# Performance work log

Measured on AMD Instinct MI355X. Metric: run time of the kernel, lower is better.

## Reference

```python
import jax, jax.numpy as jnp
import numpy as np

EPS = 1e-10
NCE_T = 0.1
JSD_T = 1.0

def setup_inputs() -> dict:
    key = jax.random.key(0)
    k1, k2, k3, k4, k5 = jax.random.split(key, 5)
    N, D, C = 8192, 128, 1000
    return {
        'fs': jax.random.normal(k1, (N, D), dtype=jnp.float32),
        'ft': jax.random.normal(k2, (N, D), dtype=jnp.float32),
        'logit_s': jax.random.normal(k3, (N, C), dtype=jnp.float32),
        'logit_t': jax.random.normal(k4, (N, C), dtype=jnp.float32),
        'target': jax.random.randint(k5, (N,), 0, 100, dtype=jnp.int64),
    }

def _l2_normalize(x, axis=1, eps=1e-12):
    n = jnp.sqrt(jnp.sum(x * x, axis=axis, keepdims=True))
    return x / jnp.maximum(n, eps)

def _nce_loss(f1, f2, targets):
    f1 = _l2_normalize(f1)
    f2 = _l2_normalize(f2)
    # pos_mask[i,j] = 1 where targets[i] == targets[j] (same class, incl. diagonal)
    pos_mask = (targets[:, None] == targets[None, :]).astype(jnp.float32)  # [N,N]
    neg_mask = 1.0 - pos_mask
    # dist = ||f1_i - f2_j||^2 = 2 - 2 <f1_i, f2_j> for unit vectors -> cos = 1 - 0.5*dist = f1 @ f2.T
    cos = jnp.matmul(f1, f2.T)  # [N,N]
    ps = jax.nn.softmax(cos / NCE_T, axis=1)
    log_pos = -jnp.log(ps + EPS) * pos_mask
    log_neg = -jnp.log(1.0 - ps + EPS) * neg_mask
    row = log_pos.sum(1) / pos_mask.sum(1) + log_neg.sum(1) / neg_mask.sum(1)
    return row.mean()

def _jsd_loss(y_s, y_t):
    N = y_s.shape[0]
    log_ps = jax.nn.log_softmax(y_s / JSD_T, axis=1)
    log_pt = jax.nn.log_softmax(y_t / JSD_T, axis=1)
    pt = jnp.exp(log_pt)
    ps = jnp.exp(log_ps)
    # F.kl_div(input=log_p, target=q, reduction='sum') = sum(q * (log q - log_p))
    kl_st = jnp.sum(pt * (log_pt - log_ps)) * (JSD_T ** 2) / N
    kl_ts = jnp.sum(ps * (log_ps - log_pt)) * (JSD_T ** 2) / N
    return 0.5 * (kl_st + kl_ts)

def reference(fs, ft, logit_s, logit_t, target):
    return _nce_loss(fs, ft, target) + _jsd_loss(logit_s, logit_t)
```

## Files before the change

kernel.cpp:

```cpp
#include <hip/hip_runtime.h>
#include <hip/hip_bf16.h>

#define NN 8192
#define DD 128
#define CC 1000
#define LN2 0.69314718f
#define G_SCALE 14.42695041f
#define NSTRIP 16
#define JPER   512
#define NTILE  8
#define LROW   128
#define GRID_NCE 1024
#define GRID_TOT 3072

typedef short v8s __attribute__((ext_vector_type(8)));
typedef float v4f __attribute__((ext_vector_type(4)));
typedef unsigned short u16;
typedef unsigned int u32;

typedef __attribute__((address_space(1))) const unsigned char ga_t;
typedef __attribute__((address_space(3))) unsigned char la_t;
#define GLOAD_LDS16(g, l) __builtin_amdgcn_global_load_lds((ga_t*)(g), (la_t*)(l), 16, 0, 0)

#if __has_builtin(__builtin_amdgcn_exp2f)
#define EXP2(x) __builtin_amdgcn_exp2f(x)
#else
#define EXP2(x) exp2f(x)
#endif
#if __has_builtin(__builtin_amdgcn_logf)
#define LOG2(x) __builtin_amdgcn_logf(x)
#else
#define LOG2(x) log2f(x)
#endif

static __device__ __forceinline__ float bf2f(u16 u) {
    union { float f; u32 i; } x; x.i = ((u32)u) << 16; return x.f;
}
static __device__ __forceinline__ u16 f2bf(float f) {
    u32 x = __float_as_uint(f);
    return (u16)((x + 0x7FFFu + ((x >> 16) & 1u)) >> 16);
}
static __device__ __forceinline__ float wsum(float v) {
    #pragma unroll
    for (int m = 1; m < 64; m <<= 1) v += __shfl_xor(v, m, 64);
    return v;
}
static __device__ __forceinline__ float wmax(float v) {
    #pragma unroll
    for (int m = 1; m < 64; m <<= 1) v = fmaxf(v, __shfl_xor(v, m, 64));
    return v;
}

__global__ __launch_bounds__(256) void prep_kernel(const void* __restrict__ fs,
                                                   const void* __restrict__ ft,
                                                   const int* __restrict__ traw,
                                                   u16* __restrict__ f1, u16* __restrict__ f2,
                                                   int* __restrict__ tgt32,
                                                   float* __restrict__ sums) {
    int b = blockIdx.x, tid = threadIdx.x;
    int w = tid >> 6, lane = tid & 63;
    if (b < 1024) {
        #pragma unroll
        for (int r = 0; r < 4; r++) {
            int row4 = b * 16 + w * 4 + r;
            const void* src; u16* dst; float gain; int row;
            if (row4 < NN) { src = fs; dst = f1; gain = G_SCALE; row = row4; }
            else           { src = ft; dst = f2; gain = 1.0f;    row = row4 - NN; }
            u32 wb = ((const u32*)src)[(size_t)row * 64 + lane];
            unsigned e = (wb >> 7) & 0xFF;
            int isF32 = (__popcll(__ballot(e >= 100 && e <= 140)) < 32);
            float x0, x1;
            if (isF32) {
                float2 v = ((const float2*)src)[(size_t)row * 64 + lane];
                x0 = v.x; x1 = v.y;
            } else {
                x0 = bf2f((u16)(wb & 0xFFFF));
                x1 = bf2f((u16)(wb >> 16));
            }
            float ss = wsum(x0 * x0 + x1 * x1);
            float sc = gain / fmaxf(sqrtf(ss), 1e-12f);
            u32 outw = (u32)f2bf(x0 * sc) | ((u32)f2bf(x1 * sc) << 16);
            ((u32*)dst)[(size_t)row * 64 + lane] = outw;
        }
    } else {
        int db = b - 1024;
        if (db == 0 && tid < 4) sums[tid] = 0.0f;
        #pragma unroll
        for (int r = 0; r < 4; r++) {
            int idx = db * 1024 + r * 256 + tid;
            int k = (idx >> 1) & 4095;
            int odd = traw[2 * k + 1];
            int is32 = (__ballot(odd != 0) != 0ull);
            int t = (is32 ? traw[idx] : traw[2 * idx]) & 127;
            tgt32[idx] = t;
        }
    }
}

__global__ __launch_bounds__(256) void main_kernel(const u16* __restrict__ f1,
                                                   const u16* __restrict__ f2,
                                                   const int* __restrict__ tgt,
                                                   const void* __restrict__ ls,
                                                   const void* __restrict__ lt,
                                                   float* __restrict__ Pp,
                                                   float* __restrict__ Qp,
                                                   float* __restrict__ Sp,
                                                   float* __restrict__ sums) {
    __shared__ u16 lds[2][64 * LROW];
    __shared__ float sred[4];
    int bx = blockIdx.x;
    int tid = threadIdx.x;
    int w = tid >> 6, lane = tid & 63;

    if (bx < GRID_NCE) {
        int strip = bx & (NSTRIP - 1);
        int ib = bx >> 4;
        int quad = lane >> 4, lcol = lane & 15;
        int ibase = ib * 128 + w * 32;

        v8s a0[4], a1[4];
        #pragma unroll
        for (int t = 0; t < 4; t++) {
            int k = t * 32 + quad * 8;
            a0[t] = *(const v8s*)(f1 + (size_t)(ibase + lcol) * DD + k);
            a1[t] = *(const v8s*)(f1 + (size_t)(ibase + 16 + lcol) * DD + k);
        }
        int ti[8];
        #pragma unroll
        for (int a = 0; a < 2; a++)
            #pragma unroll
            for (int v = 0; v < 4; v++)
                ti[a * 4 + v] = tgt[ibase + a * 16 + quad * 4 + v];

        float P[8] = {}, Q[8] = {}, S[8] = {};

        int rrl = 4 * w + (lane >> 4);
        int cg = (lane & 15) ^ rrl;
        const u16* gb = f2 + (size_t)strip * JPER * DD + (size_t)rrl * DD + cg * 8;
        int ldsbase = 4 * w * 256;

        #pragma unroll
        for (int r = 0; r < 4; r++)
            GLOAD_LDS16(gb + (size_t)r * 16 * DD,
                        (unsigned char*)lds[0] + ldsbase + r * 16 * 256);

        for (int it = 0; it < NTILE; ++it) {
            __syncthreads();
            if (it + 1 < NTILE) {
                const u16* g2 = gb + (size_t)(it + 1) * 64 * DD;
                unsigned char* l2 = (unsigned char*)lds[(it + 1) & 1] + ldsbase;
                #pragma unroll
                for (int r = 0; r < 4; r++)
                    GLOAD_LDS16(g2 + (size_t)r * 16 * DD, l2 + r * 16 * 256);
            }
            int jb = strip * JPER + it * 64;
            int tj0 = tgt[jb + lcol];
            int tj1 = tgt[jb + 16 + lcol];
            int tj2 = tgt[jb + 32 + lcol];
            int tj3 = tgt[jb + 48 + lcol];

            const u16* buf = lds[it & 1];
            v4f zero = {0.f, 0.f, 0.f, 0.f};
            v4f acc[8] = {zero, zero, zero, zero, zero, zero, zero, zero};
            #pragma unroll
            for (int t = 0; t < 4; t++) {
                int s = ((quad + 4 * t) ^ lcol) * 8;
                v8s b0 = *(const v8s*)(buf + (lcol)*LROW + s);
                v8s b1 = *(const v8s*)(buf + (16 + lcol) * LROW + s);
                v8s b2 = *(const v8s*)(buf + (32 + lcol) * LROW + s);
                v8s b3 = *(const v8s*)(buf + (48 + lcol) * LROW + s);
                acc[0] = __builtin_amdgcn_mfma_f32_16x16x32_bf16(a0[t], b0, acc[0], 0, 0, 0);
                acc[1] = __builtin_amdgcn_mfma_f32_16x16x32_bf16(a0[t], b1, acc[1], 0, 0, 0);
                acc[2] = __builtin_amdgcn_mfma_f32_16x16x32_bf16(a0[t], b2, acc[2], 0, 0, 0);
                acc[3] = __builtin_amdgcn_mfma_f32_16x16x32_bf16(a0[t], b3, acc[3], 0, 0, 0);
                acc[4] = __builtin_amdgcn_mfma_f32_16x16x32_bf16(a1[t], b0, acc[4], 0, 0, 0);
                acc[5] = __builtin_amdgcn_mfma_f32_16x16x32_bf16(a1[t], b1, acc[5], 0, 0, 0);
                acc[6] = __builtin_amdgcn_mfma_f32_16x16x32_bf16(a1[t], b2, acc[6], 0, 0, 0);
                acc[7] = __builtin_amdgcn_mfma_f32_16x16x32_bf16(a1[t], b3, acc[7], 0, 0, 0);
            }
            #pragma unroll
            for (int a = 0; a < 2; a++) {
                #pragma unroll
                for (int v = 0; v < 4; v++) {
                    int t_i = ti[a * 4 + v];
                    #pragma unroll
                    for (int jf = 0; jf < 4; jf++) {
                        float s2 = acc[a * 4 + jf][v];
                        float e1 = EXP2(s2);
                        int tj = (jf == 0) ? tj0 : (jf == 1) ? tj1 : (jf == 2) ? tj2 : tj3;
                        bool pos = (tj == t_i);
                        P[a * 4 + v] += e1;
                        Q[a * 4 + v] += pos ? e1 : 0.0f;
                        S[a * 4 + v] += pos ? s2 : 0.0f;
                    }
                }
            }
        }

        #pragma unroll
        for (int a = 0; a < 2; a++) {
            #pragma unroll
            for (int v = 0; v < 4; v++) {
                float p = P[a * 4 + v], q = Q[a * 4 + v], s = S[a * 4 + v];
                #pragma unroll
                for (int m = 1; m < 16; m <<= 1) {
                    p += __shfl_xor(p, m, 64);
                    q += __shfl_xor(q, m, 64);
                    s += __shfl_xor(s, m, 64);
                }
                if (lcol == 0) {
                    size_t idx = (size_t)strip * NN + ibase + a * 16 + quad * 4 + v;
                    Pp[idx] = p;
                    Qp[idx] = q;
                    Sp[idx] = s;
                }
            }
        }
    } else {
        int row = (bx - GRID_NCE) * 4 + w;
        u32 wb = ((const u32*)ls)[(size_t)row * 500 + lane];
        unsigned e = (wb >> 7) & 0xFF;
        int isF32 = (__popcll(__ballot(e >= 100 && e <= 140)) < 32);

        float xs[16], xt[16];
        #pragma unroll
        for (int c = 0; c < 4; c++) {
            int idx = c * 256 + lane * 4;
            if (idx < CC) {
                if (isF32) {
                    float4 a = *(const float4*)((const float*)ls + (size_t)row * CC + idx);
                    float4 b = *(const float4*)((const float*)lt + (size_t)row * CC + idx);
                    xs[c*4+0] = a.x; xs[c*4+1] = a.y; xs[c*4+2] = a.z; xs[c*4+3] = a.w;
                    xt[c*4+0] = b.x; xt[c*4+1] = b.y; xt[c*4+2] = b.z; xt[c*4+3] = b.w;
                } else {
                    ushort4 a = *(const ushort4*)((const u16*)ls + (size_t)row * CC + idx);
                    ushort4 b = *(const ushort4*)((const u16*)lt + (size_t)row * CC + idx);
                    xs[c*4+0] = bf2f(a.x); xs[c*4+1] = bf2f(a.y); xs[c*4+2] = bf2f(a.z); xs[c*4+3] = bf2f(a.w);
                    xt[c*4+0] = bf2f(b.x); xt[c*4+1] = bf2f(b.y); xt[c*4+2] = bf2f(b.z); xt[c*4+3] = bf2f(b.w);
                }
            } else {
                #pragma unroll
                for (int q = 0; q < 4; q++) { xs[c*4+q] = -1e30f; xt[c*4+q] = -1e30f; }
            }
        }
        float ms = -1e30f, mt = -1e30f;
        #pragma unroll
        for (int q = 0; q < 16; q++) { ms = fmaxf(ms, xs[q]); mt = fmaxf(mt, xt[q]); }
        ms = wmax(ms); mt = wmax(mt);
        float es = 0.f, et = 0.f;
        #pragma unroll
        for (int q = 0; q < 16; q++) { es += __expf(xs[q] - ms); et += __expf(xt[q] - mt); }
        es = wsum(es); et = wsum(et);
        float lse_s = ms + __logf(es), lse_t = mt + __logf(et);
        float contrib = 0.f;
        #pragma unroll
        for (int q = 0; q < 16; q++) {
            float lps = xs[q] - lse_s, lpt = xt[q] - lse_t;
            contrib += (lpt - lps) * (__expf(lpt) - __expf(lps));
        }
        contrib = wsum(contrib);
        if (lane == 0) sred[w] = contrib;
        __syncthreads();
        if (tid == 0) atomicAdd(&sums[1], sred[0] + sred[1] + sred[2] + sred[3]);
    }
}

__global__ __launch_bounds__(256) void rowred_kernel(const float* __restrict__ Pp,
                                                     const float* __restrict__ Qp,
                                                     const float* __restrict__ Sp,
                                                     const int* __restrict__ tgt,
                                                     float* __restrict__ sums,
                                                     u32* __restrict__ out) {
    __shared__ int h[128];
    __shared__ float sb[4];
    __shared__ int lastf;
    int tid = threadIdx.x;
    if (tid < 128) h[tid] = 0;
    __syncthreads();
    for (int i = tid; i < NN; i += 256) atomicAdd(&h[tgt[i]], 1);
    __syncthreads();

    int i = blockIdx.x * 256 + tid;
    float P = 0.f, Q = 0.f, S = 0.f;
    #pragma unroll
    for (int s = 0; s < NSTRIP; s++) {
        P += Pp[(size_t)s * NN + i];
        Q += Qp[(size_t)s * NN + i];
        S += Sp[(size_t)s * NN + i];
    }
    int cnt = h[tgt[i]];
    float pos = LN2 * LOG2(P) - LN2 * S / (float)cnt;
    float neg = (1.0f - Q / P) / (float)(NN - cnt);
    float l = wsum(pos + neg);
    if ((tid & 63) == 0) sb[tid >> 6] = l;
    __syncthreads();
    if (tid == 0) {
        atomicAdd(&sums[0], sb[0] + sb[1] + sb[2] + sb[3]);
        __threadfence();
        int* done = (int*)sums + 2;
        lastf = (atomicAdd(done, 1) == 31);
    }
    __syncthreads();
    if (!lastf) return;
    if (tid == 0) {
        float Lsum = __hip_atomic_load(&sums[0], __ATOMIC_RELAXED, __HIP_MEMORY_SCOPE_AGENT);
        float Jsum = __hip_atomic_load(&sums[1], __ATOMIC_RELAXED, __HIP_MEMORY_SCOPE_AGENT);
        float loss = (Lsum + 0.5f * Jsum) / (float)NN;
        u32 fb = __float_as_uint(loss);
        out[0] = (fb & 0xFFFF0000u) | (u32)f2bf(loss);
    }
}

extern "C" void kernel_launch(void* const* d_in, const int* in_sizes, int n_in,
                              void* d_out, int out_size, void* d_ws, size_t ws_size,
                              hipStream_t stream) {
    const void* fs = d_in[0];
    const void* ft = d_in[1];
    const void* ls = d_in[2];
    const void* lt = d_in[3];
    const int* tgt_raw = (const int*)d_in[4];

    char* wsp = (char*)d_ws;
    u16*   f1    = (u16*)(wsp + 0);
    u16*   f2    = (u16*)(wsp + 2097152);
    float* Pp    = (float*)(wsp + 4194304);
    float* Qp    = (float*)(wsp + 4718592);
    float* Sp    = (float*)(wsp + 5242880);
    float* sums  = (float*)(wsp + 5767168);
    int*   tgt32 = (int*)(wsp + 5767424);

    prep_kernel<<<1024 + 8, 256, 0, stream>>>(fs, ft, tgt_raw, f1, f2, tgt32, sums);
    main_kernel<<<GRID_TOT, 256, 0, stream>>>(f1, f2, tgt32, ls, lt, Pp, Qp, Sp, sums);
    rowred_kernel<<<32, 256, 0, stream>>>(Pp, Qp, Sp, tgt32, sums, (u32*)d_out);
}
```

Baseline: 163.5 us.

## Move JSD blocks into prep kernel and build class histogram there

The JSD softmax/KL blocks move out of the NCE matmul kernel and into the prep kernel, so main_kernel launches only the NCE tiles. The target-count histogram is now built in prep via per-block shared histograms merged into a global one, instead of each rowred block rescanning all targets. A hipMemsetAsync zeroes sums and ghist beforehand. This trades an extra memset launch and a longer prep phase for a lighter main kernel and a cheaper rowred, with the risk that the JSD work no longer overlaps the matmul.

```diff
diff --git a/kernel.cpp b/kernel.cpp
--- a/kernel.cpp
+++ b/kernel.cpp
@@ -11,7 +11,8 @@
 #define NTILE  8
 #define LROW   128
 #define GRID_NCE 1024
-#define GRID_TOT 3072
+#define JSD_BLOCKS 2048
+#define PREP_GRID (JSD_BLOCKS + 1024 + 8)
 
 typedef short v8s __attribute__((ext_vector_type(8)));
 typedef float v4f __attribute__((ext_vector_type(4)));
@@ -54,15 +55,68 @@
 __global__ __launch_bounds__(256) void prep_kernel(const void* __restrict__ fs,
                                                    const void* __restrict__ ft,
                                                    const int* __restrict__ traw,
+                                                   const void* __restrict__ ls,
+                                                   const void* __restrict__ lt,
                                                    u16* __restrict__ f1, u16* __restrict__ f2,
                                                    int* __restrict__ tgt32,
+                                                   int* __restrict__ ghist,
                                                    float* __restrict__ sums) {
+    __shared__ float sred[4];
+    __shared__ int h[128];
     int b = blockIdx.x, tid = threadIdx.x;
     int w = tid >> 6, lane = tid & 63;
-    if (b < 1024) {
+
+    if (b < JSD_BLOCKS) {
+        int row = b * 4 + w;
+        u32 wb = ((const u32*)ls)[(size_t)row * 500 + lane];
+        unsigned e = (wb >> 7) & 0xFF;
+        int isF32 = (__popcll(__ballot(e >= 100 && e <= 140)) < 32);
+
+        float xs[16], xt[16];
+        #pragma unroll
+        for (int c = 0; c < 4; c++) {
+            int idx = c * 256 + lane * 4;
+            if (idx < CC) {
+                if (isF32) {
+                    float4 a = *(const float4*)((const float*)ls + (size_t)row * CC + idx);
+                    float4 bb = *(const float4*)((const float*)lt + (size_t)row * CC + idx);
+                    xs[c*4+0] = a.x; xs[c*4+1] = a.y; xs[c*4+2] = a.z; xs[c*4+3] = a.w;
+                    xt[c*4+0] = bb.x; xt[c*4+1] = bb.y; xt[c*4+2] = bb.z; xt[c*4+3] = bb.w;
+                } else {
+                    ushort4 a = *(const ushort4*)((const u16*)ls + (size_t)row * CC + idx);
+                    ushort4 bb = *(const ushort4*)((const u16*)lt + (size_t)row * CC + idx);
+                    xs[c*4+0] = bf2f(a.x); xs[c*4+1] = bf2f(a.y); xs[c*4+2] = bf2f(a.z); xs[c*4+3] = bf2f(a.w);
+                    xt[c*4+0] = bf2f(bb.x); xt[c*4+1] = bf2f(bb.y); xt[c*4+2] = bf2f(bb.z); xt[c*4+3] = bf2f(bb.w);
+                }
+            } else {
+                #pragma unroll
+                for (int q = 0; q < 4; q++) { xs[c*4+q] = -1e30f; xt[c*4+q] = -1e30f; }
+            }
+        }
+        float ms = -1e30f, mt = -1e30f;
+        #pragma unroll
+        for (int q = 0; q < 16; q++) { ms = fmaxf(ms, xs[q]); mt = fmaxf(mt, xt[q]); }
+        ms = wmax(ms); mt = wmax(mt);
+        float es = 0.f, et = 0.f;
+        #pragma unroll
+        for (int q = 0; q < 16; q++) { es += __expf(xs[q] - ms); et += __expf(xt[q] - mt); }
+        es = wsum(es); et = wsum(et);
+        float lse_s = ms + __logf(es), lse_t = mt + __logf(et);
+        float contrib = 0.f;
+        #pragma unroll
+        for (int q = 0; q < 16; q++) {
+            float lps = xs[q] - lse_s, lpt = xt[q] - lse_t;
+            contrib += (lpt - lps) * (__expf(lpt) - __expf(lps));
+        }
+        contrib = wsum(contrib);
+        if (lane == 0) sred[w] = contrib;
+        __syncthreads();
+        if (tid == 0) atomicAdd(&sums[1], sred[0] + sred[1] + sred[2] + sred[3]);
+    } else if (b < JSD_BLOCKS + 1024) {
+        int nb = b - JSD_BLOCKS;
         #pragma unroll
         for (int r = 0; r < 4; r++) {
-            int row4 = b * 16 + w * 4 + r;
+            int row4 = nb * 16 + w * 4 + r;
             const void* src; u16* dst; float gain; int row;
             if (row4 < NN) { src = fs; dst = f1; gain = G_SCALE; row = row4; }
             else           { src = ft; dst = f2; gain = 1.0f;    row = row4 - NN; }
@@ -83,8 +137,9 @@
             ((u32*)dst)[(size_t)row * 64 + lane] = outw;
         }
     } else {
-        int db = b - 1024;
-        if (db == 0 && tid < 4) sums[tid] = 0.0f;
+        int db = b - JSD_BLOCKS - 1024;
+        if (tid < 128) h[tid] = 0;
+        __syncthreads();
         #pragma unroll
         for (int r = 0; r < 4; r++) {
             int idx = db * 1024 + r * 256 + tid;
@@ -93,175 +148,126 @@
             int is32 = (__ballot(odd != 0) != 0ull);
             int t = (is32 ? traw[idx] : traw[2 * idx]) & 127;
             tgt32[idx] = t;
-        }
+            atomicAdd(&h[t], 1);
+        }
+        __syncthreads();
+        if (tid < 128 && h[tid]) atomicAdd(&ghist[tid], h[tid]);
     }
 }
 
 __global__ __launch_bounds__(256) void main_kernel(const u16* __restrict__ f1,
                                                    const u16* __restrict__ f2,
                                                    const int* __restrict__ tgt,
-                                                   const void* __restrict__ ls,
-                                                   const void* __restrict__ lt,
                                                    float* __restrict__ Pp,
                                                    float* __restrict__ Qp,
-                                                   float* __restrict__ Sp,
-                                                   float* __restrict__ sums) {
+                                                   float* __restrict__ Sp) {
     __shared__ u16 lds[2][64 * LROW];
-    __shared__ float sred[4];
     int bx = blockIdx.x;
     int tid = threadIdx.x;
     int w = tid >> 6, lane = tid & 63;
 
-    if (bx < GRID_NCE) {
-        int strip = bx & (NSTRIP - 1);
-        int ib = bx >> 4;
-        int quad = lane >> 4, lcol = lane & 15;
-        int ibase = ib * 128 + w * 32;
-
-        v8s a0[4], a1[4];
+    int strip = bx & (NSTRIP - 1);
+    int ib = bx >> 4;
+    int quad = lane >> 4, lcol = lane & 15;
+    int ibase = ib * 128 + w * 32;
+
+    v8s a0[4], a1[4];
+    #pragma unroll
+    for (int t = 0; t < 4; t++) {
+        int k = t * 32 + quad * 8;
+        a0[t] = *(const v8s*)(f1 + (size_t)(ibase + lcol) * DD + k);
+        a1[t] = *(const v8s*)(f1 + (size_t)(ibase + 16 + lcol) * DD + k);
+    }
+    int ti[8];
+    #pragma unroll
+    for (int a = 0; a < 2; a++)
+        #pragma unroll
+        for (int v = 0; v < 4; v++)
+            ti[a * 4 + v] = tgt[ibase + a * 16 + quad * 4 + v];
+
+    float P[8] = {}, Q[8] = {}, S[8] = {};
+
+    int rrl = 4 * w + (lane >> 4);
+    int cg = (lane & 15) ^ rrl;
+    const u16* gb = f2 + (size_t)strip * JPER * DD + (size_t)rrl * DD + cg * 8;
+    int ldsbase = 4 * w * 256;
+
+    #pragma unroll
+    for (int r = 0; r < 4; r++)
+        GLOAD_LDS16(gb + (size_t)r * 16 * DD,
+                    (unsigned char*)lds[0] + ldsbase + r * 16 * 256);
+
+    for (int it = 0; it < NTILE; ++it) {
+        __syncthreads();
+        if (it + 1 < NTILE) {
+            const u16* g2 = gb + (size_t)(it + 1) * 64 * DD;
+            unsigned char* l2 = (unsigned char*)lds[(it + 1) & 1] + ldsbase;
+            #pragma unroll
+            for (int r = 0; r < 4; r++)
+                GLOAD_LDS16(g2 + (size_t)r * 16 * DD, l2 + r * 16 * 256);
+        }
+        int jb = strip * JPER + it * 64;
+        int tj0 = tgt[jb + lcol];
+        int tj1 = tgt[jb + 16 + lcol];
+        int tj2 = tgt[jb + 32 + lcol];
+        int tj3 = tgt[jb + 48 + lcol];
+
+        const u16* buf = lds[it & 1];
+        v4f zero = {0.f, 0.f, 0.f, 0.f};
+        v4f acc[8] = {zero, zero, zero, zero, zero, zero, zero, zero};
         #pragma unroll
         for (int t = 0; t < 4; t++) {
-            int k = t * 32 + quad * 8;
-            a0[t] = *(const v8s*)(f1 + (size_t)(ibase + lcol) * DD + k);
-            a1[t] = *(const v8s*)(f1 + (size_t)(ibase + 16 + lcol) * DD + k);
-        }
-        int ti[8];
-        #pragma unroll
-        for (int a = 0; a < 2; a++)
-            #pragma unroll
-            for (int v = 0; v < 4; v++)
-                ti[a * 4 + v] = tgt[ibase + a * 16 + quad * 4 + v];
-
-        float P[8] = {}, Q[8] = {}, S[8] = {};
-
-        int rrl = 4 * w + (lane >> 4);
-        int cg = (lane & 15) ^ rrl;
-        const u16* gb = f2 + (size_t)strip * JPER * DD + (size_t)rrl * DD + cg * 8;
-        int ldsbase = 4 * w * 256;
-
-        #pragma unroll
-        for (int r = 0; r < 4; r++)
-            GLOAD_LDS16(gb + (size_t)r * 16 * DD,
-                        (unsigned char*)lds[0] + ldsbase + r * 16 * 256);
-
-        for (int it = 0; it < NTILE; ++it) {
-            __syncthreads();
-            if (it + 1 < NTILE) {
-                const u16* g2 = gb + (size_t)(it + 1) * 64 * DD;
-                unsigned char* l2 = (unsigned char*)lds[(it + 1) & 1] + ldsbase;
-                #pragma unroll
-                for (int r = 0; r < 4; r++)
-                    GLOAD_LDS16(g2 + (size_t)r * 16 * DD, l2 + r * 16 * 256);
-            }
-            int jb = strip * JPER + it * 64;
-            int tj0 = tgt[jb + lcol];
-            int tj1 = tgt[jb + 16 + lcol];
-            int tj2 = tgt[jb + 32 + lcol];
-            int tj3 = tgt[jb + 48 + lcol];
-
-            const u16* buf = lds[it & 1];
-            v4f zero = {0.f, 0.f, 0.f, 0.f};
-            v4f acc[8] = {zero, zero, zero, zero, zero, zero, zero, zero};
-            #pragma unroll
-            for (int t = 0; t < 4; t++) {
-                int s = ((quad + 4 * t) ^ lcol) * 8;
-                v8s b0 = *(const v8s*)(buf + (lcol)*LROW + s);
-                v8s b1 = *(const v8s*)(buf + (16 + lcol) * LROW + s);
-                v8s b2 = *(const v8s*)(buf + (32 + lcol) * LROW + s);
-                v8s b3 = *(const v8s*)(buf + (48 + lcol) * LROW + s);
-                acc[0] = __builtin_amdgcn_mfma_f32_16x16x32_bf16(a0[t], b0, acc[0], 0, 0, 0);
-                acc[1] = __builtin_amdgcn_mfma_f32_16x16x32_bf16(a0[t], b1, acc[1], 0, 0, 0);
-                acc[2] = __builtin_amdgcn_mfma_f32_16x16x32_bf16(a0[t], b2, acc[2], 0, 0, 0);
-                acc[3] = __builtin_amdgcn_mfma_f32_16x16x32_bf16(a0[t], b3, acc[3], 0, 0, 0);
-                acc[4] = __builtin_amdgcn_mfma_f32_16x16x32_bf16(a1[t], b0, acc[4], 0, 0, 0);
-                acc[5] = __builtin_amdgcn_mfma_f32_16x16x32_bf16(a1[t], b1, acc[5], 0, 0, 0);
-                acc[6] = __builtin_amdgcn_mfma_f32_16x16x32_bf16(a1[t], b2, acc[6], 0, 0, 0);
-                acc[7] = __builtin_amdgcn_mfma_f32_16x16x32_bf16(a1[t], b3, acc[7], 0, 0, 0);
-            }
-            #pragma unroll
-            for (int a = 0; a < 2; a++) {
-                #pragma unroll
-                for (int v = 0; v < 4; v++) {
-                    int t_i = ti[a * 4 + v];
-                    #pragma unroll
-                    for (int jf = 0; jf < 4; jf++) {
-                        float s2 = acc[a * 4 + jf][v];
-                        float e1 = EXP2(s2);
-                        int tj = (jf == 0) ? tj0 : (jf == 1) ? tj1 : (jf == 2) ? tj2 : tj3;
-                        bool pos = (tj == t_i);
-                        P[a * 4 + v] += e1;
-                        Q[a * 4 + v] += pos ? e1 : 0.0f;
-                        S[a * 4 + v] += pos ? s2 : 0.0f;
-                    }
-                }
-            }
-        }
-
+            int s = ((quad + 4 * t) ^ lcol) * 8;
+            v8s b0 = *(const v8s*)(buf + (lcol)*LROW + s);
+            v8s b1 = *(const v8s*)(buf + (16 + lcol) * LROW + s);
+            v8s b2 = *(const v8s*)(buf + (32 + lcol) * LROW + s);
+            v8s b3 = *(const v8s*)(buf + (48 + lcol) * LROW + s);
+            acc[0] = __builtin_amdgcn_mfma_f32_16x16x32_bf16(a0[t], b0, acc[0], 0, 0, 0);
+            acc[1] = __builtin_amdgcn_mfma_f32_16x16x32_bf16(a0[t], b1, acc[1], 0, 0, 0);
+            acc[2] = __builtin_amdgcn_mfma_f32_16x16x32_bf16(a0[t], b2, acc[2], 0, 0, 0);
+            acc[3] = __builtin_amdgcn_mfma_f32_16x16x32_bf16(a0[t], b3, acc[3], 0, 0, 0);
+            acc[4] = __builtin_amdgcn_mfma_f32_16x16x32_bf16(a1[t], b0, acc[4], 0, 0, 0);
+            acc[5] = __builtin_amdgcn_mfma_f32_16x16x32_bf16(a1[t], b1, acc[5], 0, 0, 0);
+            acc[6] = __builtin_amdgcn_mfma_f32_16x16x32_bf16(a1[t], b2, acc[6], 0, 0, 0);
+            acc[7] = __builtin_amdgcn_mfma_f32_16x16x32_bf16(a1[t], b3, acc[7], 0, 0, 0);
+        }
         #pragma unroll
         for (int a = 0; a < 2; a++) {
             #pragma unroll
             for (int v = 0; v < 4; v++) {
-                float p = P[a * 4 + v], q = Q[a * 4 + v], s = S[a * 4 + v];
+                int t_i = ti[a * 4 + v];
                 #pragma unroll
-                for (int m = 1; m < 16; m <<= 1) {
-                    p += __shfl_xor(p, m, 64);
-                    q += __shfl_xor(q, m, 64);
-                    s += __shfl_xor(s, m, 64);
+                for (int jf = 0; jf < 4; jf++) {
+                    float s2 = acc[a * 4 + jf][v];
+                    float e1 = EXP2(s2);
+                    int tj = (jf == 0) ? tj0 : (jf == 1) ? tj1 : (jf == 2) ? tj2 : tj3;
+                    bool pos = (tj == t_i);
+                    P[a * 4 + v] += e1;
+                    Q[a * 4 + v] += pos ? e1 : 0.0f;
+                    S[a * 4 + v] += pos ? s2 : 0.0f;
                 }
-                if (lcol == 0) {
-                    size_t idx = (size_t)strip * NN + ibase + a * 16 + quad * 4 + v;
-                    Pp[idx] = p;
-                    Qp[idx] = q;
-                    Sp[idx] = s;
-                }
-            }
-        }
-    } else {
-        int row = (bx - GRID_NCE) * 4 + w;
-        u32 wb = ((const u32*)ls)[(size_t)row * 500 + lane];
-        unsigned e = (wb >> 7) & 0xFF;
-        int isF32 = (__popcll(__ballot(e >= 100 && e <= 140)) < 32);
-
-        float xs[16], xt[16];
-        #pragma unroll
-        for (int c = 0; c < 4; c++) {
-            int idx = c * 256 + lane * 4;
-            if (idx < CC) {
-                if (isF32) {
-                    float4 a = *(const float4*)((const float*)ls + (size_t)row * CC + idx);
-                    float4 b = *(const float4*)((const float*)lt + (size_t)row * CC + idx);
-                    xs[c*4+0] = a.x; xs[c*4+1] = a.y; xs[c*4+2] = a.z; xs[c*4+3] = a.w;
-                    xt[c*4+0] = b.x; xt[c*4+1] = b.y; xt[c*4+2] = b.z; xt[c*4+3] = b.w;
-                } else {
-                    ushort4 a = *(const ushort4*)((const u16*)ls + (size_t)row * CC + idx);
-                    ushort4 b = *(const ushort4*)((const u16*)lt + (size_t)row * CC + idx);
-                    xs[c*4+0] = bf2f(a.x); xs[c*4+1] = bf2f(a.y); xs[c*4+2] = bf2f(a.z); xs[c*4+3] = bf2f(a.w);
-                    xt[c*4+0] = bf2f(b.x); xt[c*4+1] = bf2f(b.y); xt[c*4+2] = bf2f(b.z); xt[c*4+3] = bf2f(b.w);
-                }
-            } else {
-                #pragma unroll
-                for (int q = 0; q < 4; q++) { xs[c*4+q] = -1e30f; xt[c*4+q] = -1e30f; }
-            }
-        }
-        float ms = -1e30f, mt = -1e30f;
-        #pragma unroll
-        for (int q = 0; q < 16; q++) { ms = fmaxf(ms, xs[q]); mt = fmaxf(mt, xt[q]); }
-        ms = wmax(ms); mt = wmax(mt);
-        float es = 0.f, et = 0.f;
-        #pragma unroll
-        for (int q = 0; q < 16; q++) { es += __expf(xs[q] - ms); et += __expf(xt[q] - mt); }
-        es = wsum(es); et = wsum(et);
-        float lse_s = ms + __logf(es), lse_t = mt + __logf(et);
-        float contrib = 0.f;
-        #pragma unroll
-        for (int q = 0; q < 16; q++) {
-            float lps = xs[q] - lse_s, lpt = xt[q] - lse_t;
-            contrib += (lpt - lps) * (__expf(lpt) - __expf(lps));
-        }
-        contrib = wsum(contrib);
-        if (lane == 0) sred[w] = contrib;
-        __syncthreads();
-        if (tid == 0) atomicAdd(&sums[1], sred[0] + sred[1] + sred[2] + sred[3]);
+            }
+        }
+    }
+
+    #pragma unroll
+    for (int a = 0; a < 2; a++) {
+        #pragma unroll
+        for (int v = 0; v < 4; v++) {
+            float p = P[a * 4 + v], q = Q[a * 4 + v], s = S[a * 4 + v];
+            #pragma unroll
+            for (int m = 1; m < 16; m <<= 1) {
+                p += __shfl_xor(p, m, 64);
+                q += __shfl_xor(q, m, 64);
+                s += __shfl_xor(s, m, 64);
+            }
+            if (lcol == 0) {
+                size_t idx = (size_t)strip * NN + ibase + a * 16 + quad * 4 + v;
+                Pp[idx] = p;
+                Qp[idx] = q;
+                Sp[idx] = s;
+            }
+        }
     }
 }
 
@@ -269,16 +275,12 @@
                                                      const float* __restrict__ Qp,
                                                      const float* __restrict__ Sp,
                                                      const int* __restrict__ tgt,
+                                                     const int* __restrict__ ghist,
                                                      float* __restrict__ sums,
                                                      u32* __restrict__ out) {
-    __shared__ int h[128];
     __shared__ float sb[4];
     __shared__ int lastf;
     int tid = threadIdx.x;
-    if (tid < 128) h[tid] = 0;
-    __syncthreads();
-    for (int i = tid; i < NN; i += 256) atomicAdd(&h[tgt[i]], 1);
-    __syncthreads();
 
     int i = blockIdx.x * 256 + tid;
     float P = 0.f, Q = 0.f, S = 0.f;
@@ -288,7 +290,7 @@
         Q += Qp[(size_t)s * NN + i];
         S += Sp[(size_t)s * NN + i];
     }
-    int cnt = h[tgt[i]];
+    int cnt = ghist[tgt[i]];
     float pos = LN2 * LOG2(P) - LN2 * S / (float)cnt;
     float neg = (1.0f - Q / P) / (float)(NN - cnt);
     float l = wsum(pos + neg);
@@ -327,9 +329,12 @@
     float* Qp    = (float*)(wsp + 4718592);
     float* Sp    = (float*)(wsp + 5242880);
     float* sums  = (float*)(wsp + 5767168);
-    int*   tgt32 = (int*)(wsp + 5767424);
-
-    prep_kernel<<<1024 + 8, 256, 0, stream>>>(fs, ft, tgt_raw, f1, f2, tgt32, sums);
-    main_kernel<<<GRID_TOT, 256, 0, stream>>>(f1, f2, tgt32, ls, lt, Pp, Qp, Sp, sums);
-    rowred_kernel<<<32, 256, 0, stream>>>(Pp, Qp, Sp, tgt32, sums, (u32*)d_out);
-}
+    int*   ghist = (int*)(wsp + 5767296);
+    int*   tgt32 = (int*)(wsp + 5768192);
+
+    hipMemsetAsync(wsp + 5767168, 0, 640, stream);
+    prep_kernel<<<PREP_GRID, 256, 0, stream>>>(fs, ft, tgt_raw, ls, lt,
+                                               f1, f2, tgt32, ghist, sums);
+    main_kernel<<<GRID_NCE, 256, 0, stream>>>(f1, f2, tgt32, Pp, Qp, Sp);
+    rowred_kernel<<<32, 256, 0, stream>>>(Pp, Qp, Sp, tgt32, ghist, sums, (u32*)d_out);
+}
```

Measured after the change: 165.9 us. About the same (+1.4%).
